# Performance work log

Hardware: AMD Instinct MI355X
Metric: run time of the kernel (lower is better)

Reference implementation:

```python
import jax, jax.numpy as jnp
import numpy as np

N_NODES = 50000
N_EDGES = 800000
IN_DIM = 128
HID_DIM = 128
NUM_GRAPHS = 64


def gcn_conv(x, edge_index, W, b):
    """PyG GCNConv: symmetric-normalized aggregation with self-loops.
    out = D^{-1/2} (A + I) D^{-1/2} (x @ W) + b
    """
    n = x.shape[0]
    loop = jnp.arange(n, dtype=edge_index.dtype)
    src = jnp.concatenate([edge_index[0], loop])  # [E+N]
    dst = jnp.concatenate([edge_index[1], loop])
    deg = jax.ops.segment_sum(jnp.ones_like(dst, x.dtype), dst, num_segments=n)
    dinv = jnp.where(deg > 0, jax.lax.rsqrt(deg), 0.0)
    norm = dinv[src] * dinv[dst]  # [E+N]
    h = x @ W  # [N, H] transform before propagate (PyG order)
    msg = h[src] * norm[:, None]  # [E+N, H] gathered+scaled messages
    out = jax.ops.segment_sum(msg, dst, num_segments=n)  # scatter-add
    return out + b


def global_mean_pool(x, batch, num_graphs):
    s = jax.ops.segment_sum(x, batch, num_segments=num_graphs)
    cnt = jax.ops.segment_sum(jnp.ones((x.shape[0],), x.dtype), batch, num_segments=num_graphs)
    return s / jnp.maximum(cnt, 1.0)[:, None]


def setup_inputs() -> dict:
    key = jax.random.key(0)
    ks = jax.random.split(key, 8)
    x = jax.random.normal(ks[0], (N_NODES, IN_DIM), dtype=jnp.float32)
    edge_index = jax.random.randint(ks[1], (2, N_EDGES), 0, N_NODES, dtype=jnp.int64)
    batch = jnp.sort(jax.random.randint(ks[2], (N_NODES,), 0, NUM_GRAPHS, dtype=jnp.int64))
    s1 = 1.0 / np.sqrt(IN_DIM)
    s2 = 1.0 / np.sqrt(HID_DIM)
    W1 = jax.random.uniform(ks[3], (IN_DIM, HID_DIM), jnp.float32, -s1, s1)
    b1 = jnp.zeros((HID_DIM,), jnp.float32)
    W2 = jax.random.uniform(ks[4], (HID_DIM, HID_DIM), jnp.float32, -s2, s2)
    b2 = jnp.zeros((HID_DIM,), jnp.float32)
    Wc = jax.random.uniform(ks[5], (HID_DIM, 1), jnp.float32, -s2, s2)
    bc = jnp.zeros((1,), jnp.float32)
    return {"x": x, "edge_index": edge_index, "batch": batch,
            "W1": W1, "b1": b1, "W2": W2, "b2": b2, "Wc": Wc, "bc": bc}


def reference(x, edge_index, batch, W1, b1, W2, b2, Wc, bc):
    h = jax.nn.relu(gcn_conv(x, edge_index, W1, b1))
    # dropout p=0.1 is identity in eval mode
    h = gcn_conv(h, edge_index, W2, b2)
    g = global_mean_pool(h, batch, NUM_GRAPHS)  # [G, H]
    return jax.nn.sigmoid(g @ Wc + bc)  # [G, 1]
```

## Files before the change

kernel.cpp:

```cpp
#include <hip/hip_runtime.h>
#include <hip/hip_bf16.h>
#include <hip/hip_fp16.h>

#define N_NODES 50000
#define N_EDGES 800000
#define DIM     128
#define NG      64
#define GN      16
#define CAP     48
#define AGG_EB  256
#define LAXP    136

#define FILL_B  3125
#define CAST_B  1563
#define VB_B    129
#define WF_B    8

typedef float  f2_t  __attribute__((ext_vector_type(2)));
typedef float  f32x4 __attribute__((ext_vector_type(4)));
typedef _Float16 f16x8 __attribute__((ext_vector_type(8)));
typedef _Float16 f16x4 __attribute__((ext_vector_type(4)));

__global__ void k_prep(const int* __restrict__ ei, int* __restrict__ cur,
                       unsigned int* __restrict__ csr,
                       const float4* __restrict__ x4, uint4* __restrict__ xq4,
                       const float* __restrict__ W2, const float* __restrict__ Wc,
                       const float* __restrict__ b2, float* __restrict__ v,
                       float* __restrict__ beta2,
                       const float* __restrict__ W1, f16x8* __restrict__ w1f) {
    __shared__ float red[4];
    int bid = blockIdx.x, t = threadIdx.x;
    if (bid < FILL_B) {
        int e = bid * 256 + t;
        int s = ei[e];
        int d = ei[N_EDGES + e];
        int pos = atomicAdd(&cur[d], 1);
        if (pos < CAP) csr[d * CAP + pos] = (unsigned)s;
    } else if (bid < FILL_B + CAST_B) {
        int idx = (bid - FILL_B) * 256 + t;
        if (idx < N_NODES * DIM / 16) {
            uint4 o;
            unsigned* op = (unsigned*)&o;
            #pragma unroll
            for (int q = 0; q < 4; q++) {
                float4 f = x4[idx * 4 + q];
                int p = 0;
                p = __builtin_amdgcn_cvt_pk_fp8_f32(f.x, f.y, p, false);
                p = __builtin_amdgcn_cvt_pk_fp8_f32(f.z, f.w, p, true);
                op[q] = (unsigned)p;
            }
            xq4[idx] = o;
        }
    } else if (bid < FILL_B + CAST_B + VB_B) {
        int b = bid - (FILL_B + CAST_B);
        float p = 0.f;
        if (t < DIM) p = (b < DIM) ? W2[b * DIM + t] * Wc[t] : b2[t] * Wc[t];
        #pragma unroll
        for (int off = 32; off > 0; off >>= 1) p += __shfl_down(p, off, 64);
        if ((t & 63) == 0) red[t >> 6] = p;
        __syncthreads();
        if (t == 0) {
            float s = red[0] + red[1];
            if (b < DIM) v[b] = s; else beta2[0] = s;
        }
    } else {
        int idx = (bid - (FILL_B + CAST_B + VB_B)) * 256 + t;
        int ntile = idx >> 8, kb = (idx >> 6) & 3, l = idx & 63;
        int kbase = kb * 32 + (l >> 4) * 8;
        int n = ntile * 16 + (l & 15);
        f16x8 o;
        #pragma unroll
        for (int j = 0; j < 8; j++) o[j] = (_Float16)W1[(kbase + j) * DIM + n];
        w1f[idx] = o;
    }
}

__global__ void k_stamp(const int* __restrict__ cur, unsigned int* __restrict__ csr) {
    int idx = blockIdx.x * 256 + threadIdx.x;
    if (idx >= N_NODES * CAP) return;
    int n = idx / CAP;
    int slot = idx - n * CAP;
    int deg = min(cur[n], CAP);
    if (slot < deg) {
        unsigned e = csr[idx] & 0xFFFFu;
        float w = rsqrtf((float)cur[e] + 1.f);
        unsigned hw = (unsigned)__half_as_ushort(__float2half(w));
        csr[idx] = e | (hw << 16);
    }
}

__global__ __launch_bounds__(512) void k_node(
    const unsigned int* __restrict__ xq,
    const unsigned int* __restrict__ csr,
    const f16x8* __restrict__ w1f,
    const float* __restrict__ b1,
    const float* __restrict__ v, const int* __restrict__ cur,
    float* __restrict__ z2) {
    __shared__ _Float16 laxh[GN * LAXP];
    __shared__ float redm[GN * 8];
    int tid = threadIdx.x;
    int w = tid >> 6, l = tid & 63;
    int half = l >> 5, hl = l & 31;
    int node0 = blockIdx.x * GN;

    {
        int i = node0 + 2 * w + half;
        int start = i * CAP;
        int len = min(cur[i], CAP);
        int lm1 = (len > 0) ? len - 1 : 0;
        float di = rsqrtf((float)cur[i] + 1.f);

        unsigned su = xq[(size_t)i * 32 + hl];
        f2_t s01 = __builtin_amdgcn_cvt_pk_f32_fp8((int)su, false);
        f2_t s23 = __builtin_amdgcn_cvt_pk_f32_fp8((int)su, true);
        float a0 = di * s01.x, a1 = di * s01.y;
        float a2 = di * s23.x, a3 = di * s23.y;
        float b0 = 0.f, b1_ = 0.f, b2_ = 0.f, b3 = 0.f;
        float c0 = 0.f, c1 = 0.f, c2 = 0.f, c3 = 0.f;
        float d0 = 0.f, d1 = 0.f, d2 = 0.f, d3 = 0.f;

        int lenmax = max(len, __shfl_xor(len, 32, 64));
        for (int j = 0; j < lenmax; j += 4) {
            int j0 = min(j + 0, lm1), j1 = min(j + 1, lm1);
            int j2 = min(j + 2, lm1), j3 = min(j + 3, lm1);
            unsigned p0 = csr[start + j0];
            unsigned p1 = csr[start + j1];
            unsigned p2 = csr[start + j2];
            unsigned p3 = csr[start + j3];
            float w0 = (j + 0 < len) ? __half2float(__ushort_as_half((unsigned short)(p0 >> 16))) : 0.f;
            float w1 = (j + 1 < len) ? __half2float(__ushort_as_half((unsigned short)(p1 >> 16))) : 0.f;
            float w2 = (j + 2 < len) ? __half2float(__ushort_as_half((unsigned short)(p2 >> 16))) : 0.f;
            float w3 = (j + 3 < len) ? __half2float(__ushort_as_half((unsigned short)(p3 >> 16))) : 0.f;
            unsigned q0 = xq[(size_t)(p0 & 0xFFFFu) * 32 + hl];
            unsigned q1 = xq[(size_t)(p1 & 0xFFFFu) * 32 + hl];
            unsigned q2 = xq[(size_t)(p2 & 0xFFFFu) * 32 + hl];
            unsigned q3 = xq[(size_t)(p3 & 0xFFFFu) * 32 + hl];
            f2_t e01, e23;
            e01 = __builtin_amdgcn_cvt_pk_f32_fp8((int)q0, false);
            e23 = __builtin_amdgcn_cvt_pk_f32_fp8((int)q0, true);
            a0 = fmaf(w0, e01.x, a0); a1 = fmaf(w0, e01.y, a1);
            a2 = fmaf(w0, e23.x, a2); a3 = fmaf(w0, e23.y, a3);
            e01 = __builtin_amdgcn_cvt_pk_f32_fp8((int)q1, false);
            e23 = __builtin_amdgcn_cvt_pk_f32_fp8((int)q1, true);
            b0 = fmaf(w1, e01.x, b0); b1_ = fmaf(w1, e01.y, b1_);
            b2_ = fmaf(w1, e23.x, b2_); b3 = fmaf(w1, e23.y, b3);
            e01 = __builtin_amdgcn_cvt_pk_f32_fp8((int)q2, false);
            e23 = __builtin_amdgcn_cvt_pk_f32_fp8((int)q2, true);
            c0 = fmaf(w2, e01.x, c0); c1 = fmaf(w2, e01.y, c1);
            c2 = fmaf(w2, e23.x, c2); c3 = fmaf(w2, e23.y, c3);
            e01 = __builtin_amdgcn_cvt_pk_f32_fp8((int)q3, false);
            e23 = __builtin_amdgcn_cvt_pk_f32_fp8((int)q3, true);
            d0 = fmaf(w3, e01.x, d0); d1 = fmaf(w3, e01.y, d1);
            d2 = fmaf(w3, e23.x, d2); d3 = fmaf(w3, e23.y, d3);
        }
        a0 += b0 + c0 + d0; a1 += b1_ + c1 + d1;
        a2 += b2_ + c2 + d2; a3 += b3 + c3 + d3;
        f16x4 pk;
        pk[0] = (_Float16)(di * a0); pk[1] = (_Float16)(di * a1);
        pk[2] = (_Float16)(di * a2); pk[3] = (_Float16)(di * a3);
        *(f16x4*)&laxh[(2 * w + half) * LAXP + 4 * hl] = pk;
    }
    __syncthreads();

    f32x4 acc = {0.f, 0.f, 0.f, 0.f};
    #pragma unroll
    for (int kb = 0; kb < 4; kb++) {
        f16x8 af = *(const f16x8*)&laxh[(l & 15) * LAXP + kb * 32 + (l >> 4) * 8];
        f16x8 bf = w1f[(w * 4 + kb) * 64 + l];
        acc = __builtin_amdgcn_mfma_f32_16x16x32_f16(af, bf, acc, 0, 0, 0);
    }
    int n = w * 16 + (l & 15);
    float bn = b1[n], vn = v[n];
    #pragma unroll
    for (int r = 0; r < 4; r++) {
        float p = fmaxf(acc[r] + bn, 0.f) * vn;
        p += __shfl_xor(p, 1, 64);
        p += __shfl_xor(p, 2, 64);
        p += __shfl_xor(p, 4, 64);
        p += __shfl_xor(p, 8, 64);
        if ((l & 15) == 0) redm[((l >> 4) * 4 + r) * 8 + w] = p;
    }
    __syncthreads();
    if (tid < GN) {
        float s = 0.f;
        #pragma unroll
        for (int q = 0; q < 8; q++) s += redm[tid * 8 + q];
        z2[node0 + tid] = rsqrtf((float)cur[node0 + tid] + 1.f) * s;
    }
}

__global__ void k_aggz(const float* __restrict__ z2, const int* __restrict__ cur,
                       const int* __restrict__ ei, const int* __restrict__ batch,
                       float* __restrict__ gpartE, float* __restrict__ gpartN,
                       int* __restrict__ gcnt) {
    int bid = blockIdx.x, t = threadIdx.x;
    if (bid < AGG_EB) {
        __shared__ float bs[4][NG];
        bs[t >> 6][t & 63] = 0.f;
        __syncthreads();
        int wg = t >> 6;
        for (int base = bid * 1024; base < N_EDGES; base += AGG_EB * 1024) {
            #pragma unroll
            for (int k = 0; k < 4; k++) {
                int e = base + k * 256 + t;
                if (e < N_EDGES) {
                    int s = ei[e];
                    int d = ei[N_EDGES + e];
                    float dv = rsqrtf((float)cur[d] + 1.f);
                    atomicAdd(&bs[wg][batch[d]], dv * z2[s]);
                }
            }
        }
        __syncthreads();
        if (t < NG) gpartE[bid * NG + t] = bs[0][t] + bs[1][t] + bs[2][t] + bs[3][t];
    } else {
        __shared__ int range[2];
        __shared__ float rs[4];
        int g = bid - AGG_EB;
        if (t < 2) {
            int key = g + t;
            int lo = 0, hi = N_NODES;
            while (lo < hi) { int m = (lo + hi) >> 1; if (batch[m] < key) lo = m + 1; else hi = m; }
            range[t] = lo;
        }
        __syncthreads();
        int lo = range[0], hi = range[1];
        float loc = 0.f;
        for (int i = lo + t; i < hi; i += 256)
            loc += rsqrtf((float)cur[i] + 1.f) * z2[i];
        #pragma unroll
        for (int off = 32; off > 0; off >>= 1) loc += __shfl_down(loc, off, 64);
        if ((t & 63) == 0) rs[t >> 6] = loc;
        __syncthreads();
        if (t == 0) {
            gpartN[g] = rs[0] + rs[1] + rs[2] + rs[3];
            gcnt[g] = hi - lo;
        }
    }
}

__global__ void k_final(const float* __restrict__ gpartE, const float* __restrict__ gpartN,
                        const int* __restrict__ gcnt, const float* __restrict__ beta2,
                        const float* __restrict__ bcin, float* __restrict__ out) {
    __shared__ float acc[4][NG];
    int t = threadIdx.x;
    int g = t & 63, c = t >> 6;
    float s = 0.f;
    for (int k = 0; k < AGG_EB / 4; k++)
        s += gpartE[(c * (AGG_EB / 4) + k) * NG + g];
    acc[c][g] = s;
    __syncthreads();
    if (t < NG) {
        float tot = acc[0][t] + acc[1][t] + acc[2][t] + acc[3][t] + gpartN[t];
        int cnt = gcnt[t];
        float val = tot / (float)(cnt > 0 ? cnt : 1) + beta2[0] + bcin[0];
        out[t] = 1.f / (1.f + expf(-val));
    }
}

extern "C" void kernel_launch(void* const* d_in, const int* in_sizes, int n_in,
                              void* d_out, int out_size, void* d_ws, size_t ws_size,
                              hipStream_t stream) {
    const float* x   = (const float*)d_in[0];
    const int*   ei  = (const int*)  d_in[1];
    const int*   bat = (const int*)  d_in[2];
    const float* W1  = (const float*)d_in[3];
    const float* b1  = (const float*)d_in[4];
    const float* W2  = (const float*)d_in[5];
    const float* b2  = (const float*)d_in[6];
    const float* Wc  = (const float*)d_in[7];
    const float* bc  = (const float*)d_in[8];
    float* out = (float*)d_out;

    char* w = (char*)d_ws;
    size_t off = 0;
    auto alloc = [&](size_t bytes) -> void* {
        void* p = w + off;
        off = (off + bytes + 255) & ~(size_t)255;
        return p;
    };
    int*   cur     = (int*)  alloc(N_NODES * 4);
    size_t zero_len = off;
    float* z2      = (float*)alloc(N_NODES * 4);
    float* v       = (float*)alloc(DIM * 4);
    float* beta2   = (float*)alloc(4);
    float* gpartE  = (float*)alloc((size_t)AGG_EB * NG * 4);
    float* gpartN  = (float*)alloc(NG * 4);
    int*   gcnt    = (int*)  alloc(NG * 4);
    f16x8* w1f     = (f16x8*)alloc(2048 * 16);
    unsigned int* xq  = (unsigned int*)alloc((size_t)N_NODES * DIM);
    unsigned int* csr = (unsigned int*)alloc((size_t)N_NODES * CAP * 4);
    (void)ws_size; (void)in_sizes; (void)n_in; (void)out_size;

    hipMemsetAsync(d_ws, 0, zero_len, stream);

    dim3 b256(256);
    k_prep<<<dim3(FILL_B + CAST_B + VB_B + WF_B), b256, 0, stream>>>(
        ei, cur, csr, (const float4*)x, (uint4*)xq, W2, Wc, b2, v, beta2, W1, w1f);
    k_stamp<<<dim3((N_NODES * CAP + 255) / 256), b256, 0, stream>>>(cur, csr);
    k_node<<<dim3(N_NODES / GN), dim3(512), 0, stream>>>(
        xq, csr, w1f, b1, v, cur, z2);
    k_aggz<<<dim3(AGG_EB + NG), b256, 0, stream>>>(z2, cur, ei, bat, gpartE, gpartN, gcnt);
    k_final<<<dim3(1), b256, 0, stream>>>(gpartE, gpartN, gcnt, beta2, bc, out);
}
```

Baseline: 183.4 us.

## Build CSR via two-level binned counting sort instead of global atomics

Replaces the per-edge global atomicAdd CSR fill and the stamping pass with a binned counting sort. Edges are histogrammed into 256-node bins, a prefix scan gives bin offsets, edges are scattered into bins, and then per-bin kernels compute degrees and fill the CSR slots with LDS atomics while stamping normalization weights. The aim is to avoid contended random global atomics and the full-array stamp sweep over N*CAP slots. In exchange it adds three extra launches, an extra pass over the edge list, and an 800K-entry intermediate buffer.

```diff
diff --git a/kernel.cpp b/kernel.cpp
--- a/kernel.cpp
+++ b/kernel.cpp
@@ -11,7 +11,10 @@
 #define AGG_EB  256
 #define LAXP    136
 
-#define FILL_B  3125
+#define NBIN    196
+#define SORT_B  250
+#define EPB     3200
+
 #define CAST_B  1563
 #define VB_B    129
 #define WF_B    8
@@ -21,23 +24,30 @@
 typedef _Float16 f16x8 __attribute__((ext_vector_type(8)));
 typedef _Float16 f16x4 __attribute__((ext_vector_type(4)));
 
-__global__ void k_prep(const int* __restrict__ ei, int* __restrict__ cur,
-                       unsigned int* __restrict__ csr,
+__global__ void k_prep(const int* __restrict__ ei, int* __restrict__ binCnt,
                        const float4* __restrict__ x4, uint4* __restrict__ xq4,
                        const float* __restrict__ W2, const float* __restrict__ Wc,
                        const float* __restrict__ b2, float* __restrict__ v,
                        float* __restrict__ beta2,
                        const float* __restrict__ W1, f16x8* __restrict__ w1f) {
     __shared__ float red[4];
+    __shared__ int hist[256];
     int bid = blockIdx.x, t = threadIdx.x;
-    if (bid < FILL_B) {
-        int e = bid * 256 + t;
-        int s = ei[e];
-        int d = ei[N_EDGES + e];
-        int pos = atomicAdd(&cur[d], 1);
-        if (pos < CAP) csr[d * CAP + pos] = (unsigned)s;
-    } else if (bid < FILL_B + CAST_B) {
-        int idx = (bid - FILL_B) * 256 + t;
+    if (bid < SORT_B) {
+        hist[t] = 0;
+        __syncthreads();
+        int base = bid * EPB;
+        for (int r = 0; r < 13; r++) {
+            int idx = r * 256 + t;
+            if (idx < EPB) {
+                int d = ei[N_EDGES + base + idx];
+                atomicAdd(&hist[d >> 8], 1);
+            }
+        }
+        __syncthreads();
+        if (t < NBIN && hist[t] > 0) atomicAdd(&binCnt[t], hist[t]);
+    } else if (bid < SORT_B + CAST_B) {
+        int idx = (bid - SORT_B) * 256 + t;
         if (idx < N_NODES * DIM / 16) {
             uint4 o;
             unsigned* op = (unsigned*)&o;
@@ -51,8 +61,8 @@
             }
             xq4[idx] = o;
         }
-    } else if (bid < FILL_B + CAST_B + VB_B) {
-        int b = bid - (FILL_B + CAST_B);
+    } else if (bid < SORT_B + CAST_B + VB_B) {
+        int b = bid - (SORT_B + CAST_B);
         float p = 0.f;
         if (t < DIM) p = (b < DIM) ? W2[b * DIM + t] * Wc[t] : b2[t] * Wc[t];
         #pragma unroll
@@ -64,7 +74,7 @@
             if (b < DIM) v[b] = s; else beta2[0] = s;
         }
     } else {
-        int idx = (bid - (FILL_B + CAST_B + VB_B)) * 256 + t;
+        int idx = (bid - (SORT_B + CAST_B + VB_B)) * 256 + t;
         int ntile = idx >> 8, kb = (idx >> 6) & 3, l = idx & 63;
         int kbase = kb * 32 + (l >> 4) * 8;
         int n = ntile * 16 + (l & 15);
@@ -75,17 +85,91 @@
     }
 }
 
-__global__ void k_stamp(const int* __restrict__ cur, unsigned int* __restrict__ csr) {
-    int idx = blockIdx.x * 256 + threadIdx.x;
-    if (idx >= N_NODES * CAP) return;
-    int n = idx / CAP;
-    int slot = idx - n * CAP;
-    int deg = min(cur[n], CAP);
-    if (slot < deg) {
-        unsigned e = csr[idx] & 0xFFFFu;
-        float w = rsqrtf((float)cur[e] + 1.f);
-        unsigned hw = (unsigned)__half_as_ushort(__float2half(w));
-        csr[idx] = e | (hw << 16);
+__global__ void k_scan(const int* __restrict__ binCnt, int* __restrict__ binOff,
+                       int* __restrict__ binCur) {
+    __shared__ int s[256];
+    int t = threadIdx.x;
+    int c = (t < NBIN) ? binCnt[t] : 0;
+    s[t] = c;
+    #pragma unroll
+    for (int off = 1; off < 256; off <<= 1) {
+        __syncthreads();
+        int v2 = (t >= off) ? s[t - off] : 0;
+        __syncthreads();
+        s[t] += v2;
+    }
+    __syncthreads();
+    if (t < NBIN) {
+        int excl = s[t] - c;
+        binOff[t] = excl;
+        binCur[t] = excl;
+    }
+}
+
+__global__ void k_scatter(const int* __restrict__ ei, int* __restrict__ binCur,
+                          unsigned int* __restrict__ sorted) {
+    __shared__ int hist[256];
+    __shared__ int cur[256];
+    int bid = blockIdx.x, t = threadIdx.x;
+    hist[t] = 0;
+    __syncthreads();
+    int base = bid * EPB;
+    for (int r = 0; r < 13; r++) {
+        int idx = r * 256 + t;
+        if (idx < EPB) {
+            int d = ei[N_EDGES + base + idx];
+            atomicAdd(&hist[d >> 8], 1);
+        }
+    }
+    __syncthreads();
+    if (t < NBIN && hist[t] > 0) cur[t] = atomicAdd(&binCur[t], hist[t]);
+    __syncthreads();
+    for (int r = 0; r < 13; r++) {
+        int idx = r * 256 + t;
+        if (idx < EPB) {
+            int e = base + idx;
+            int s = ei[e];
+            int d = ei[N_EDGES + e];
+            int pos = atomicAdd(&cur[d >> 8], 1);
+            sorted[pos] = (unsigned)s | ((unsigned)(d & 255) << 16);
+        }
+    }
+}
+
+__global__ void k_deg(const unsigned int* __restrict__ sorted,
+                      const int* __restrict__ binOff, int* __restrict__ deg) {
+    __shared__ int cnt[256];
+    int b = blockIdx.x, t = threadIdx.x;
+    cnt[t] = 0;
+    __syncthreads();
+    int lo = binOff[b];
+    int hi = (b == NBIN - 1) ? N_EDGES : binOff[b + 1];
+    for (int i = lo + t; i < hi; i += 256)
+        atomicAdd(&cnt[sorted[i] >> 16], 1);
+    __syncthreads();
+    int node = b * 256 + t;
+    if (node < N_NODES) deg[node] = cnt[t];
+}
+
+__global__ void k_build(const unsigned int* __restrict__ sorted,
+                        const int* __restrict__ binOff, const int* __restrict__ deg,
+                        unsigned int* __restrict__ csr) {
+    __shared__ int cur[256];
+    int b = blockIdx.x, t = threadIdx.x;
+    cur[t] = 0;
+    __syncthreads();
+    int lo = binOff[b];
+    int hi = (b == NBIN - 1) ? N_EDGES : binOff[b + 1];
+    for (int i = lo + t; i < hi; i += 256) {
+        unsigned e = sorted[i];
+        unsigned src = e & 0xFFFFu;
+        unsigned dLow = e >> 16;
+        int pos = atomicAdd(&cur[dLow], 1);
+        if (pos < CAP) {
+            float w = rsqrtf((float)deg[src] + 1.f);
+            unsigned hw = (unsigned)__half_as_ushort(__float2half(w));
+            csr[(b * 256 + dLow) * CAP + pos] = src | (hw << 16);
+        }
     }
 }
 
@@ -94,7 +178,7 @@
     const unsigned int* __restrict__ csr,
     const f16x8* __restrict__ w1f,
     const float* __restrict__ b1,
-    const float* __restrict__ v, const int* __restrict__ cur,
+    const float* __restrict__ v, const int* __restrict__ deg,
     float* __restrict__ z2) {
     __shared__ _Float16 laxh[GN * LAXP];
     __shared__ float redm[GN * 8];
@@ -106,9 +190,9 @@
     {
         int i = node0 + 2 * w + half;
         int start = i * CAP;
-        int len = min(cur[i], CAP);
+        int len = min(deg[i], CAP);
         int lm1 = (len > 0) ? len - 1 : 0;
-        float di = rsqrtf((float)cur[i] + 1.f);
+        float di = rsqrtf((float)deg[i] + 1.f);
 
         unsigned su = xq[(size_t)i * 32 + hl];
         f2_t s01 = __builtin_amdgcn_cvt_pk_f32_fp8((int)su, false);
@@ -185,11 +269,11 @@
         float s = 0.f;
         #pragma unroll
         for (int q = 0; q < 8; q++) s += redm[tid * 8 + q];
-        z2[node0 + tid] = rsqrtf((float)cur[node0 + tid] + 1.f) * s;
-    }
-}
-
-__global__ void k_aggz(const float* __restrict__ z2, const int* __restrict__ cur,
+        z2[node0 + tid] = rsqrtf((float)deg[node0 + tid] + 1.f) * s;
+    }
+}
+
+__global__ void k_aggz(const float* __restrict__ z2, const int* __restrict__ deg,
                        const int* __restrict__ ei, const int* __restrict__ batch,
                        float* __restrict__ gpartE, float* __restrict__ gpartN,
                        int* __restrict__ gcnt) {
@@ -206,7 +290,7 @@
                 if (e < N_EDGES) {
                     int s = ei[e];
                     int d = ei[N_EDGES + e];
-                    float dv = rsqrtf((float)cur[d] + 1.f);
+                    float dv = rsqrtf((float)deg[d] + 1.f);
                     atomicAdd(&bs[wg][batch[d]], dv * z2[s]);
                 }
             }
@@ -227,7 +311,7 @@
         int lo = range[0], hi = range[1];
         float loc = 0.f;
         for (int i = lo + t; i < hi; i += 256)
-            loc += rsqrtf((float)cur[i] + 1.f) * z2[i];
+            loc += rsqrtf((float)deg[i] + 1.f) * z2[i];
         #pragma unroll
         for (int off = 32; off > 0; off >>= 1) loc += __shfl_down(loc, off, 64);
         if ((t & 63) == 0) rs[t >> 6] = loc;
@@ -279,8 +363,11 @@
         off = (off + bytes + 255) & ~(size_t)255;
         return p;
     };
-    int*   cur     = (int*)  alloc(N_NODES * 4);
+    int*   binCnt  = (int*)  alloc(NBIN * 4);
     size_t zero_len = off;
+    int*   binOff  = (int*)  alloc(NBIN * 4);
+    int*   binCur  = (int*)  alloc(NBIN * 4);
+    int*   deg     = (int*)  alloc(N_NODES * 4);
     float* z2      = (float*)alloc(N_NODES * 4);
     float* v       = (float*)alloc(DIM * 4);
     float* beta2   = (float*)alloc(4);
@@ -288,18 +375,22 @@
     float* gpartN  = (float*)alloc(NG * 4);
     int*   gcnt    = (int*)  alloc(NG * 4);
     f16x8* w1f     = (f16x8*)alloc(2048 * 16);
-    unsigned int* xq  = (unsigned int*)alloc((size_t)N_NODES * DIM);
-    unsigned int* csr = (unsigned int*)alloc((size_t)N_NODES * CAP * 4);
+    unsigned int* xq     = (unsigned int*)alloc((size_t)N_NODES * DIM);
+    unsigned int* sorted = (unsigned int*)alloc((size_t)N_EDGES * 4);
+    unsigned int* csr    = (unsigned int*)alloc((size_t)N_NODES * CAP * 4);
     (void)ws_size; (void)in_sizes; (void)n_in; (void)out_size;
 
     hipMemsetAsync(d_ws, 0, zero_len, stream);
 
     dim3 b256(256);
-    k_prep<<<dim3(FILL_B + CAST_B + VB_B + WF_B), b256, 0, stream>>>(
-        ei, cur, csr, (const float4*)x, (uint4*)xq, W2, Wc, b2, v, beta2, W1, w1f);
-    k_stamp<<<dim3((N_NODES * CAP + 255) / 256), b256, 0, stream>>>(cur, csr);
+    k_prep<<<dim3(SORT_B + CAST_B + VB_B + WF_B), b256, 0, stream>>>(
+        ei, binCnt, (const float4*)x, (uint4*)xq, W2, Wc, b2, v, beta2, W1, w1f);
+    k_scan<<<dim3(1), b256, 0, stream>>>(binCnt, binOff, binCur);
+    k_scatter<<<dim3(SORT_B), b256, 0, stream>>>(ei, binCur, sorted);
+    k_deg<<<dim3(NBIN), b256, 0, stream>>>(sorted, binOff, deg);
+    k_build<<<dim3(NBIN), b256, 0, stream>>>(sorted, binOff, deg, csr);
     k_node<<<dim3(N_NODES / GN), dim3(512), 0, stream>>>(
-        xq, csr, w1f, b1, v, cur, z2);
-    k_aggz<<<dim3(AGG_EB + NG), b256, 0, stream>>>(z2, cur, ei, bat, gpartE, gpartN, gcnt);
+        xq, csr, w1f, b1, v, deg, z2);
+    k_aggz<<<dim3(AGG_EB + NG), b256, 0, stream>>>(z2, deg, ei, bat, gpartE, gpartN, gcnt);
     k_final<<<dim3(1), b256, 0, stream>>>(gpartE, gpartN, gcnt, beta2, bc, out);
 }
```

After: 172.3 us. 1.06x faster.
